# Optimization experiments

Measured on AMD Instinct MI355X. Metric: run time of the kernel, lower is better.

Reference implementation:

```python
import jax, jax.numpy as jnp
import numpy as np

INV_SQRT2 = 0.7071067811865476  # 1/sqrt(2), orthonormal Haar
N_LEVELS = 3


def setup_inputs() -> dict:
    key = jax.random.key(0)
    ks = jax.random.split(key, 5)
    B, S, D = 16, 4096, 512
    x = jax.random.normal(ks[0], (B, S, D), dtype=jnp.float32)
    sizes = [256, 128, 64]  # detail-band sizes for 3-level DWT of 512
    Wd0 = jax.random.normal(ks[1], (sizes[0], sizes[0]), dtype=jnp.float32) * 0.02
    Wd1 = jax.random.normal(ks[2], (sizes[1], sizes[1]), dtype=jnp.float32) * 0.02
    Wd2 = jax.random.normal(ks[3], (sizes[2], sizes[2]), dtype=jnp.float32) * 0.02
    Wa = jax.random.normal(ks[4], (sizes[2], sizes[2]), dtype=jnp.float32) * 0.02
    return {
        'x': x,
        'Wd0': Wd0, 'bd0': jnp.zeros((sizes[0],), jnp.float32),
        'Wd1': Wd1, 'bd1': jnp.zeros((sizes[1],), jnp.float32),
        'Wd2': Wd2, 'bd2': jnp.zeros((sizes[2],), jnp.float32),
        'Wa': Wa, 'ba': jnp.zeros((sizes[2],), jnp.float32),
    }


def reference(x, Wd0, bd0, Wd1, bd1, Wd2, bd2, Wa, ba):
    # Multi-level Haar DWT along the feature axis.
    details = []
    a = x
    for _ in range(N_LEVELS):
        e = a[..., 0::2]
        o = a[..., 1::2]
        details.append((e - o) * INV_SQRT2)  # detail coefficients
        a = (e + o) * INV_SQRT2              # approximation coefficients

    # Per-level small linear transforms (torch Linear: y = x @ W.T + b).
    Wds, bds = [Wd0, Wd1, Wd2], [bd0, bd1, bd2]
    details = [details[i] @ Wds[i].T + bds[i] for i in range(N_LEVELS)]
    a = a @ Wa.T + ba

    # Inverse Haar DWT (orthonormal): even=(a+d)/sqrt2, odd=(a-d)/sqrt2, interleave.
    for i in reversed(range(N_LEVELS)):
        d = details[i]
        e = (a + d) * INV_SQRT2
        o = (a - d) * INV_SQRT2
        a = jnp.stack([e, o], axis=-1).reshape(a.shape[:-1] + (a.shape[-1] * 2,))
    return a
```

## Files before the change

kernel.cpp:

```cpp
#include <hip/hip_runtime.h>
#include <stdint.h>

typedef float  f32x4  __attribute__((ext_vector_type(4)));
typedef short  bf16x8 __attribute__((ext_vector_type(8)));
typedef int    i32x4  __attribute__((ext_vector_type(4)));
typedef unsigned int u32x2 __attribute__((ext_vector_type(2)));

#define C1f 0.70710678118654752f
#define C2f 0.5f
#define C3f 0.35355339059327373f

#define NT 512
#define CH 32
#define RB 1040
#define CHSZ (CH*RB)
#define RPB 256
#define NCHUNK (RPB/CH)

__device__ __forceinline__ unsigned int f2b(float f) {
    unsigned int u; __builtin_memcpy(&u, &f, 4);
    u += 0x7fffu + ((u >> 16) & 1u);
    return u >> 16;
}
__device__ __forceinline__ unsigned int pack2(float lo, float hi) {
    return f2b(lo) | (f2b(hi) << 16);
}
__device__ __forceinline__ bf16x8 cast8(i32x4 v) {
    bf16x8 r; __builtin_memcpy(&r, &v, 16); return r;
}

__device__ __forceinline__ void lds_barrier() {
    asm volatile("s_waitcnt lgkmcnt(0)" ::: "memory");
    __builtin_amdgcn_s_barrier();
    __builtin_amdgcn_sched_barrier(0);
}
__device__ __forceinline__ void vwait4() {
    asm volatile("s_waitcnt vmcnt(4)" ::: "memory");
    __builtin_amdgcn_sched_barrier(0);
}

__device__ __forceinline__ bf16x8 g_frag(int o, int i0,
        const float* __restrict__ W0, const float* __restrict__ W1,
        const float* __restrict__ W2, const float* __restrict__ Wa)
{
    const float s0o = (o & 1) ? -1.f : 1.f;
    const float s1o = ((o >> 1) & 1) ? -1.f : 1.f;
    const float s2o = ((o >> 2) & 1) ? -1.f : 1.f;
    const float4 w0 = *(const float4*)(W0 + (o >> 1) * 256 + (i0 >> 1));
    const float2 w1 = *(const float2*)(W1 + (o >> 2) * 128 + (i0 >> 2));
    const float  w2 = W2[(o >> 3) * 64 + (i0 >> 3)];
    const float  wa = Wa[(o >> 3) * 64 + (i0 >> 3)];
    const float base = 0.125f * wa;
    const float c2   = 0.125f * s2o * w2;
    const float c1   = 0.25f  * s1o;
    const float c0   = 0.5f   * s0o;
    const float w0a[4] = { w0.x, w0.y, w0.z, w0.w };
    const float w1a[2] = { w1.x, w1.y };
    float g[8];
    #pragma unroll
    for (int e = 0; e < 8; ++e) {
        const float t2 = ((e >> 2) & 1) ? -c2 : c2;
        const float t1 = (((e >> 1) & 1) ? -c1 : c1) * w1a[e >> 2];
        const float t0 = ((e & 1) ? -c0 : c0) * w0a[e >> 1];
        g[e] = base + t2 + t1 + t0;
    }
    i32x4 p = { (int)pack2(g[0],g[1]), (int)pack2(g[2],g[3]),
                (int)pack2(g[4],g[5]), (int)pack2(g[6],g[7]) };
    return cast8(p);
}

__global__ void prep(const float* __restrict__ W0, const float* __restrict__ b0,
                     const float* __restrict__ W1, const float* __restrict__ b1,
                     const float* __restrict__ W2, const float* __restrict__ b2,
                     const float* __restrict__ Wa, const float* __restrict__ ba,
                     unsigned short* __restrict__ ws)
{
    const int gid  = blockIdx.x * 256 + threadIdx.x;
    const int blob = gid >> 6, lane = gid & 63;
    const int otg  = blob >> 4, ks = blob & 15;
    const int o  = otg * 16 + (lane & 15);
    const int i0 = ks * 32 + ((lane >> 4) * 8);
    bf16x8 f = g_frag(o, i0, W0, W1, W2, Wa);
    i32x4 p; __builtin_memcpy(&p, &f, 16);
    *(i32x4*)(ws + blob * 512 + lane * 8) = p;
    if (gid < 512) {
        float* gv = (float*)(ws + 262144);
        const int oo = gid;
        const float s0 = (oo & 1) ? -C1f : C1f;
        const float s1 = ((oo >> 1) & 1) ? -C2f : C2f;
        const float s2 = ((oo >> 2) & 1) ? -C3f : C3f;
        gv[oo] = C3f * ba[oo >> 3] + s2 * b2[oo >> 3] + s1 * b1[oo >> 2] + s0 * b0[oo >> 1];
    }
}

template<int USE_WS>
__global__ __launch_bounds__(NT, 2)
void wavelet_gemm(const float* __restrict__ x,
                  const float* __restrict__ W0, const float* __restrict__ b0,
                  const float* __restrict__ W1, const float* __restrict__ b1,
                  const float* __restrict__ W2, const float* __restrict__ b2,
                  const float* __restrict__ Wa, const float* __restrict__ ba,
                  const unsigned short* __restrict__ wsb,
                  float* __restrict__ out, int nblk)
{
    __shared__ char lds[2 * CHSZ];

    const int tid  = threadIdx.x;
    const int lane = tid & 63;
    const int wave = tid >> 6;

    const int cpx = nblk >> 3;
    const int lbid = ((int)blockIdx.x & 7) * cpx + ((int)blockIdx.x >> 3);
    const int chalf = lbid & 1;
    const long rowblk = (long)(lbid >> 1) * RPB;

    const int otg0 = chalf * 16 + wave * 2;
    const int col0 = otg0 * 16;
    const int bc0  = col0 + ((lane >> 4) << 2);

    bf16x8 B0[16], B1[16];
    if (USE_WS) {
        #pragma unroll
        for (int ks = 0; ks < 16; ++ks) {
            B0[ks] = cast8(*(const i32x4*)(wsb + ((size_t)(otg0 * 16 + ks) * 512) + lane * 8));
            B1[ks] = cast8(*(const i32x4*)(wsb + ((size_t)((otg0 + 1) * 16 + ks) * 512) + lane * 8));
        }
    } else {
        #pragma unroll
        for (int ks = 0; ks < 16; ++ks) {
            B0[ks] = g_frag(col0 + (lane & 15),      ks * 32 + ((lane >> 4) * 8), W0, W1, W2, Wa);
            B1[ks] = g_frag(col0 + 16 + (lane & 15), ks * 32 + ((lane >> 4) * 8), W0, W1, W2, Wa);
        }
    }
    #pragma unroll
    for (int ks = 0; ks < 16; ++ks) {
        i32x4 t0, t1;
        __builtin_memcpy(&t0, &B0[ks], 16);
        __builtin_memcpy(&t1, &B1[ks], 16);
        asm volatile("" : "+v"(t0), "+v"(t1));
        __builtin_memcpy(&B0[ks], &t0, 16);
        __builtin_memcpy(&B1[ks], &t1, 16);
    }

    f32x4 gv40, gv41;
    if (USE_WS) {
        const float4 g0 = *(const float4*)((const float*)(wsb + 262144) + bc0);
        const float4 g1 = *(const float4*)((const float*)(wsb + 262144) + bc0 + 16);
        gv40 = f32x4{ g0.x, g0.y, g0.z, g0.w };
        gv41 = f32x4{ g1.x, g1.y, g1.z, g1.w };
    } else {
        #pragma unroll
        for (int j = 0; j < 4; ++j) {
            #pragma unroll
            for (int t = 0; t < 2; ++t) {
                const int col = bc0 + t * 16 + j;
                const float s0 = (col & 1) ? -C1f : C1f;
                const float s1 = ((col >> 1) & 1) ? -C2f : C2f;
                const float s2 = ((col >> 2) & 1) ? -C3f : C3f;
                const float v = C3f * ba[col >> 3] + s2 * b2[col >> 3] + s1 * b1[col >> 2] + s0 * b0[col >> 1];
                if (t == 0) gv40[j] = v; else gv41[j] = v;
            }
        }
    }

    auto ldx = [&](int c, f32x4* v) {
        const f32x4* xb = (const f32x4*)(x + (rowblk + (long)c * CH) * 512);
        #pragma unroll
        for (int i = 0; i < 8; ++i) v[i] = xb[i * NT + tid];
    };
    auto stx = [&](int c, const f32x4* v) {
        char* base = lds + (c & 1) * CHSZ;
        #pragma unroll
        for (int i = 0; i < 8; ++i) {
            const int f = i * NT + tid;
            const int row = f >> 7, c4 = f & 127;
            u32x2 p = { pack2(v[i][0], v[i][1]), pack2(v[i][2], v[i][3]) };
            *(u32x2*)(base + row * RB + c4 * 8) = p;
        }
    };
    auto compute = [&](int c) {
        const char* base = lds + (c & 1) * CHSZ + (lane & 15) * RB + ((lane >> 4) * 16);
        const long r0 = rowblk + (long)c * CH + (lane & 15);
        #pragma unroll
        for (int m = 0; m < 2; ++m) {
            const char* pa = base + m * 16 * RB;
            f32x4 acc0 = {}, acc1 = {};
            #pragma unroll
            for (int ks = 0; ks < 16; ++ks) {
                bf16x8 a = cast8(*(const i32x4*)(pa + ks * 64));
                acc0 = __builtin_amdgcn_mfma_f32_16x16x32_bf16(B0[ks], a, acc0, 0, 0, 0);
                acc1 = __builtin_amdgcn_mfma_f32_16x16x32_bf16(B1[ks], a, acc1, 0, 0, 0);
            }
            const long rr = (r0 + m * 16) * 512;
            *(f32x4*)(out + rr + bc0)      = acc0 + gv40;
            *(f32x4*)(out + rr + bc0 + 16) = acc1 + gv41;
        }
    };

    {
        f32x4 v[8];
        ldx(0, v);
        stx(0, v);
    }
    lds_barrier();

    #pragma unroll 1
    for (int c = 0; c < NCHUNK; ++c) {
        f32x4 vn[8];
        if (c + 1 < NCHUNK) {
            ldx(c + 1, vn);
            __builtin_amdgcn_sched_barrier(0);
        }
        compute(c);
        if (c + 1 < NCHUNK) {
            vwait4();
            stx(c + 1, vn);
        }
        lds_barrier();
    }
}

extern "C" void kernel_launch(void* const* d_in, const int* in_sizes, int n_in,
                              void* d_out, int out_size, void* d_ws, size_t ws_size,
                              hipStream_t stream)
{
    const float* x  = (const float*)d_in[0];
    const float* W0 = (const float*)d_in[1];
    const float* b0 = (const float*)d_in[2];
    const float* W1 = (const float*)d_in[3];
    const float* b1 = (const float*)d_in[4];
    const float* W2 = (const float*)d_in[5];
    const float* b2 = (const float*)d_in[6];
    const float* Wa = (const float*)d_in[7];
    const float* ba = (const float*)d_in[8];
    float* out = (float*)d_out;

    const int nrows = in_sizes[0] / 512;
    const int nblk  = (nrows / RPB) * 2;

    if (ws_size >= (size_t)(524288 + 2048)) {
        unsigned short* ws = (unsigned short*)d_ws;
        prep<<<128, 256, 0, stream>>>(W0, b0, W1, b1, W2, b2, Wa, ba, ws);
        wavelet_gemm<1><<<nblk, NT, 0, stream>>>(x, W0, b0, W1, b1, W2, b2, Wa, ba, ws, out, nblk);
    } else {
        wavelet_gemm<0><<<nblk, NT, 0, stream>>>(x, W0, b0, W1, b1, W2, b2, Wa, ba, nullptr, out, nblk);
    }
}
```

Measured before the change: 75.72 us.

## Stage x into LDS via direct global-to-LDS loads with a 4-buffer pipeline

```diff
diff --git a/kernel.cpp b/kernel.cpp
--- a/kernel.cpp
+++ b/kernel.cpp
@@ -4,16 +4,16 @@
 typedef float  f32x4  __attribute__((ext_vector_type(4)));
 typedef short  bf16x8 __attribute__((ext_vector_type(8)));
 typedef int    i32x4  __attribute__((ext_vector_type(4)));
-typedef unsigned int u32x2 __attribute__((ext_vector_type(2)));
 
 #define C1f 0.70710678118654752f
 #define C2f 0.5f
 #define C3f 0.35355339059327373f
 
 #define NT 512
-#define CH 32
-#define RB 1040
-#define CHSZ (CH*RB)
+#define CH 16
+#define RBF 2064
+#define CHSZ (CH*RBF)
+#define NBUF 4
 #define RPB 256
 #define NCHUNK (RPB/CH)
 
@@ -28,15 +28,23 @@
 __device__ __forceinline__ bf16x8 cast8(i32x4 v) {
     bf16x8 r; __builtin_memcpy(&r, &v, 16); return r;
 }
+__device__ __forceinline__ unsigned int cvtpk(float lo, float hi) {
+    unsigned int r;
+    asm("v_cvt_pk_bf16_f32 %0, %1, %2" : "=v"(r) : "v"(lo), "v"(hi));
+    return r;
+}
 
 __device__ __forceinline__ void lds_barrier() {
     asm volatile("s_waitcnt lgkmcnt(0)" ::: "memory");
     __builtin_amdgcn_s_barrier();
     __builtin_amdgcn_sched_barrier(0);
 }
-__device__ __forceinline__ void vwait4() {
-    asm volatile("s_waitcnt vmcnt(4)" ::: "memory");
-    __builtin_amdgcn_sched_barrier(0);
+__device__ __forceinline__ void vwait4() { asm volatile("s_waitcnt vmcnt(4)" ::: "memory"); __builtin_amdgcn_sched_barrier(0); }
+__device__ __forceinline__ void vwait6() { asm volatile("s_waitcnt vmcnt(6)" ::: "memory"); __builtin_amdgcn_sched_barrier(0); }
+__device__ __forceinline__ void vwait8() { asm volatile("s_waitcnt vmcnt(8)" ::: "memory"); __builtin_amdgcn_sched_barrier(0); }
+
+__device__ __forceinline__ void gld_lds16(const float* g, char* l) {
+    __builtin_amdgcn_global_load_lds((const unsigned int*)g, (unsigned int*)l, 16, 0, 0);
 }
 
 __device__ __forceinline__ bf16x8 g_frag(int o, int i0,
@@ -103,7 +111,7 @@
                   const unsigned short* __restrict__ wsb,
                   float* __restrict__ out, int nblk)
 {
-    __shared__ char lds[2 * CHSZ];
+    __shared__ char lds[NBUF * CHSZ];
 
     const int tid  = threadIdx.x;
     const int lane = tid & 63;
@@ -163,60 +171,53 @@
         }
     }
 
-    auto ldx = [&](int c, f32x4* v) {
-        const f32x4* xb = (const f32x4*)(x + (rowblk + (long)c * CH) * 512);
-        #pragma unroll
-        for (int i = 0; i < 8; ++i) v[i] = xb[i * NT + tid];
-    };
-    auto stx = [&](int c, const f32x4* v) {
-        char* base = lds + (c & 1) * CHSZ;
-        #pragma unroll
-        for (int i = 0; i < 8; ++i) {
-            const int f = i * NT + tid;
-            const int row = f >> 7, c4 = f & 127;
-            u32x2 p = { pack2(v[i][0], v[i][1]), pack2(v[i][2], v[i][3]) };
-            *(u32x2*)(base + row * RB + c4 * 8) = p;
-        }
+    auto stage = [&](int c) {
+        char* base = lds + (c & (NBUF - 1)) * CHSZ;
+        const float* xc = x + (rowblk + (long)c * CH) * 512;
+        #pragma unroll
+        for (int i = 0; i < 2; ++i) {
+            const int r = wave * 2 + i;
+            const float* gp = xc + (long)r * 512 + lane * 4;
+            char* lp = base + r * RBF;
+            gld_lds16(gp, lp);
+            gld_lds16(gp + 256, lp + 1024);
+        }
+        __builtin_amdgcn_sched_barrier(0);
     };
     auto compute = [&](int c) {
-        const char* base = lds + (c & 1) * CHSZ + (lane & 15) * RB + ((lane >> 4) * 16);
-        const long r0 = rowblk + (long)c * CH + (lane & 15);
-        #pragma unroll
-        for (int m = 0; m < 2; ++m) {
-            const char* pa = base + m * 16 * RB;
-            f32x4 acc0 = {}, acc1 = {};
-            #pragma unroll
-            for (int ks = 0; ks < 16; ++ks) {
-                bf16x8 a = cast8(*(const i32x4*)(pa + ks * 64));
-                acc0 = __builtin_amdgcn_mfma_f32_16x16x32_bf16(B0[ks], a, acc0, 0, 0, 0);
-                acc1 = __builtin_amdgcn_mfma_f32_16x16x32_bf16(B1[ks], a, acc1, 0, 0, 0);
-            }
-            const long rr = (r0 + m * 16) * 512;
-            *(f32x4*)(out + rr + bc0)      = acc0 + gv40;
-            *(f32x4*)(out + rr + bc0 + 16) = acc1 + gv41;
-        }
+        const char* pa = lds + (c & (NBUF - 1)) * CHSZ + (lane & 15) * RBF + ((lane >> 4) * 32);
+        f32x4 acc0 = {}, acc1 = {};
+        #pragma unroll
+        for (int ks = 0; ks < 16; ++ks) {
+            f32x4 lo = *(const f32x4*)(pa + ks * 128);
+            f32x4 hi = *(const f32x4*)(pa + ks * 128 + 16);
+            i32x4 pk = { (int)cvtpk(lo[0], lo[1]), (int)cvtpk(lo[2], lo[3]),
+                         (int)cvtpk(hi[0], hi[1]), (int)cvtpk(hi[2], hi[3]) };
+            bf16x8 a = cast8(pk);
+            acc0 = __builtin_amdgcn_mfma_f32_16x16x32_bf16(B0[ks], a, acc0, 0, 0, 0);
+            acc1 = __builtin_amdgcn_mfma_f32_16x16x32_bf16(B1[ks], a, acc1, 0, 0, 0);
+        }
+        const long rr = (rowblk + (long)c * CH + (lane & 15)) * 512;
+        *(f32x4*)(out + rr + bc0)      = acc0 + gv40;
+        *(f32x4*)(out + rr + bc0 + 16) = acc1 + gv41;
     };
 
-    {
-        f32x4 v[8];
-        ldx(0, v);
-        stx(0, v);
-    }
+    stage(0);
+    stage(1);
+    vwait4();
     lds_barrier();
 
     #pragma unroll 1
     for (int c = 0; c < NCHUNK; ++c) {
-        f32x4 vn[8];
-        if (c + 1 < NCHUNK) {
-            ldx(c + 1, vn);
-            __builtin_amdgcn_sched_barrier(0);
-        }
+        if (c + 2 < NCHUNK) stage(c + 2);
         compute(c);
-        if (c + 1 < NCHUNK) {
+        if (c + 2 < NCHUNK) {
+            if (c == 0) vwait6(); else vwait8();
+            lds_barrier();
+        } else if (c + 1 < NCHUNK) {
             vwait4();
-            stx(c + 1, vn);
-        }
-        lds_barrier();
+            lds_barrier();
+        }
     }
 }
 
```

Measured after the change: 75.79 us. Within noise of the previous version (+0.1%).
